# Kernel optimization log

Measured on AMD Instinct MI355X. Metric: run time of the kernel, lower is better.

Reference implementation:

```python
import jax, jax.numpy as jnp
import numpy as np

GENRES = 20; TAGS = 1000; GTAGS = 1128; MOVIES = 20000; YEARS = 120; TBINS = 128
B = 1024; HIST = 50; PH = 256; OD = 128
EG = 8; ET = 16; EGT = 16; EM = 32; EY = 8; EUG = 32; ETS = 4
PAD = MOVIES  # padding index; context buffers have MOVIES+1 rows, last row = zeros


def setup_inputs():
    ks = iter(jax.random.split(jax.random.key(0), 64))
    nrm = lambda shp, s=0.1: (s * jax.random.normal(next(ks), shp)).astype(jnp.float32)
    P = MOVIES + 1
    genome_ctx = jax.random.uniform(next(ks), (P, GTAGS), dtype=jnp.float32).at[-1].set(0.0)
    genre_ctx = jax.random.uniform(next(ks), (P, GENRES), dtype=jnp.float32).at[-1].set(0.0)
    tag_ctx = jax.random.uniform(next(ks), (P, TAGS), dtype=jnp.float32).at[-1].set(0.0)
    year_ctx = jax.random.randint(next(ks), (P,), 0, YEARS).at[-1].set(0)
    return dict(
        user_genre_contexts=jax.random.uniform(next(ks), (B, GENRES), dtype=jnp.float32),
        user_watch_history=jax.random.randint(next(ks), (B, HIST), 0, P),
        user_watch_history_ratings=5.0 * jax.random.uniform(next(ks), (B, HIST), dtype=jnp.float32),
        timestamps=jax.random.randint(next(ks), (B,), 0, TBINS),
        target_movieId=jax.random.randint(next(ks), (B,), 0, MOVIES),
        genome_ctx=genome_ctx, genre_ctx=genre_ctx, tag_ctx=tag_ctx, year_ctx=year_ctx,
        item_emb=nrm((P, EM), 0.01).at[-1].set(0.0),  # padding_idx row zeroed
        year_emb_tab=nrm((YEARS, EY), 0.01),
        ts_emb_tab=nrm((TBINS, ETS), 0.01),
        w_item=nrm((EM, EM)), b_item=jnp.zeros((EM,), jnp.float32),
        w_genre=nrm((GENRES, EG)), b_genre=jnp.zeros((EG,), jnp.float32),
        w_tag=nrm((TAGS, ET)), b_tag=jnp.zeros((ET,), jnp.float32),
        w_genome=nrm((GTAGS, EGT)), b_genome=jnp.zeros((EGT,), jnp.float32),
        w_year=nrm((EY, EY)), b_year=jnp.zeros((EY,), jnp.float32),
        w_ugenre=nrm((GENRES, EUG)), b_ugenre=jnp.zeros((EUG,), jnp.float32),
        w_ts=nrm((ETS, ETS)), b_ts=jnp.zeros((ETS,), jnp.float32),
        w_up1=nrm((OD + EGT + EUG + ETS, PH)), b_up1=jnp.zeros((PH,), jnp.float32),
        w_up2=nrm((PH, OD)), b_up2=jnp.zeros((OD,), jnp.float32),
        w_ip1=nrm((EG + ET + EGT + EM + EY, PH)), b_ip1=jnp.zeros((PH,), jnp.float32),
        w_ip2=nrm((PH, OD)), b_ip2=jnp.zeros((OD,), jnp.float32),
    )


def reference(user_genre_contexts, user_watch_history, user_watch_history_ratings,
              timestamps, target_movieId, genome_ctx, genre_ctx, tag_ctx, year_ctx,
              item_emb, year_emb_tab, ts_emb_tab,
              w_item, b_item, w_genre, b_genre, w_tag, b_tag, w_genome, b_genome,
              w_year, b_year, w_ugenre, b_ugenre, w_ts, b_ts,
              w_up1, b_up1, w_up2, b_up2, w_ip1, b_ip1, w_ip2, b_ip2):
    lt = lambda x, W, b: jnp.tanh(x @ W + b)

    def item_tower(mg, mt, mgt, yr, ids):
        # concat of five small Linear+Tanh towers, then 2-layer projection MLP
        cat = jnp.concatenate([
            lt(mg, w_genre, b_genre), lt(mt, w_tag, b_tag), lt(mgt, w_genome, b_genome),
            lt(item_emb[ids], w_item, b_item), lt(year_emb_tab[yr], w_year, b_year)], axis=-1)
        return jax.nn.relu(cat @ w_ip1 + b_ip1) @ w_ip2 + b_ip2

    Bn, Hn = user_watch_history.shape
    pad_mask = (user_watch_history != PAD).astype(jnp.float32)[..., None]       # (B,H,1)
    rating_weights = user_watch_history_ratings[..., None] * pad_mask            # (B,H,1)
    weight_sum = jnp.clip(jnp.abs(rating_weights).sum(axis=1), 1e-6)             # (B,1)

    # item pool: full item-tower embeddings of watched movies, rating-weighted avg
    flat = user_watch_history.reshape(-1)
    embs = item_tower(genre_ctx[flat], tag_ctx[flat], genome_ctx[flat],
                      year_ctx[flat], flat).reshape(Bn, Hn, OD)
    item_pool = (embs * rating_weights).sum(axis=1) / weight_sum                 # (B,OD)

    # genome pool (kept separately in use_item_pool_for_history mode)
    genome_embs = lt(genome_ctx[user_watch_history], w_genome, b_genome)         # (B,H,EGT)
    genome_emb = (genome_embs * rating_weights).sum(axis=1) / weight_sum

    genre_emb = lt(user_genre_contexts, w_ugenre, b_ugenre)
    ts_emb = lt(ts_emb_tab[timestamps], w_ts, b_ts)
    user_cat = jnp.concatenate([item_pool, genome_emb, genre_emb, ts_emb], axis=1)
    user = jax.nn.relu(user_cat @ w_up1 + b_up1) @ w_up2 + b_up2                 # (B,OD)

    item = item_tower(genre_ctx[target_movieId], tag_ctx[target_movieId],
                      genome_ctx[target_movieId], year_ctx[target_movieId], target_movieId)
    return jnp.einsum('bd,bd->b', user, item)
```

## Files before the change

kernel.cpp:

```cpp
#include <hip/hip_runtime.h>
#include <hip/hip_bf16.h>

typedef __bf16 bf16x8 __attribute__((ext_vector_type(8)));
typedef __bf16 bf16x4 __attribute__((ext_vector_type(4)));
typedef float  f32x4  __attribute__((ext_vector_type(4)));

namespace {
constexpr int P       = 20001;
constexpr int NT_TILE = 1251;
constexpr int PROWS   = NT_TILE * 16;
constexpr int NGENRES = 20;
constexpr int NTAGS   = 1000;
constexpr int NGTAGS  = 1128;
constexpr int NB      = 1024;
constexpr int NH      = 50;
constexpr int PHID    = 256;
constexpr int OD      = 128;
constexpr int EG = 8, ET = 16, EGT = 16, EM = 32, EY = 8, EUG = 32, ETS = 4;
constexpr int PAD  = 20000;
constexpr int SC   = 104;
constexpr int SH   = 264;
constexpr int UC   = 192;
constexpr int UCS  = 200;
constexpr int KC_TAG = 32, KC_GEN = 36;
constexpr int KC_IP1 = 3,  NT_IP1 = 16;
constexpr int KC_IP2 = 8,  NT_IP2 = 8;
constexpr int KC_UP1 = 6,  NT_UP1 = 16;
constexpr int KC_UP2 = 8,  NT_UP2 = 8;
}

static __device__ __forceinline__ f32x4 mfma16(bf16x8 a, bf16x8 b, f32x4 c) {
  return __builtin_amdgcn_mfma_f32_16x16x32_bf16(a, b, c, 0, 0, 0);
}

static __device__ __forceinline__ bf16x8 cvt8(float4 v0, float4 v1) {
  return (bf16x8){(__bf16)v0.x, (__bf16)v0.y, (__bf16)v0.z, (__bf16)v0.w,
                  (__bf16)v1.x, (__bf16)v1.y, (__bf16)v1.z, (__bf16)v1.w};
}

__global__ __launch_bounds__(512) void setup_wf_kernel(
    const float* __restrict__ w_tag, const float* __restrict__ w_genome,
    const float* __restrict__ w_ip1, const float* __restrict__ w_ip2,
    const float* __restrict__ w_up1, const float* __restrict__ w_up2,
    __bf16* __restrict__ Wtf, __bf16* __restrict__ Wgf,
    __bf16* __restrict__ Wip1f, __bf16* __restrict__ Wip2f,
    __bf16* __restrict__ Wup1f, __bf16* __restrict__ Wup2f)
{
  const int b = blockIdx.x, t = threadIdx.x;
  const int l = t >> 3, j = t & 7;
  const int krow = (l >> 4) * 8 + j, l15 = l & 15;
  const float* src; __bf16* dst; int K, N, kc, nt;
  if (b < 32)        { src = w_tag;    dst = Wtf   + (long)b * 512;       K = NTAGS;  N = 16;  kc = b;      nt = 0; }
  else if (b < 68)   { int i = b - 32;  src = w_genome; dst = Wgf   + (long)i * 512; K = NGTAGS; N = 16;  kc = i;      nt = 0; }
  else if (b < 116)  { int i = b - 68;  src = w_ip1;    dst = Wip1f + (long)i * 512; K = 80;     N = 256; kc = i / 16; nt = i % 16; }
  else if (b < 180)  { int i = b - 116; src = w_ip2;    dst = Wip2f + (long)i * 512; K = 256;    N = 128; kc = i / 8;  nt = i % 8; }
  else if (b < 276)  { int i = b - 180; src = w_up1;    dst = Wup1f + (long)i * 512; K = 180;    N = 256; kc = i / 16; nt = i % 16; }
  else               { int i = b - 276; src = w_up2;    dst = Wup2f + (long)i * 512; K = 256;    N = 128; kc = i / 8;  nt = i % 8; }
  const int k = kc * 32 + krow, n = nt * 16 + l15;
  float v = (k < K) ? src[(long)k * N + n] : 0.f;
  dst[t] = (__bf16)v;
}

__global__ __launch_bounds__(256, 3) void tower_kernel(
    const float* __restrict__ tag_ctx, const float* __restrict__ genome_ctx,
    const float* __restrict__ genre_ctx, const int* __restrict__ year_ctx,
    const float* __restrict__ item_emb, const float* __restrict__ year_tab,
    const float* __restrict__ w_genre, const float* __restrict__ b_genre,
    const float* __restrict__ b_tag,   const float* __restrict__ b_genome,
    const float* __restrict__ w_item,  const float* __restrict__ b_item,
    const float* __restrict__ w_year,  const float* __restrict__ b_year,
    const float* __restrict__ b_ip1,   const float* __restrict__ b_ip2,
    const __bf16* __restrict__ Wtf,   const __bf16* __restrict__ Wgf,
    const __bf16* __restrict__ Wip1f, const __bf16* __restrict__ Wip2f,
    float* __restrict__ T, float* __restrict__ GT)
{
  __shared__ __align__(16) __bf16 s_cat[16][SC];
  __shared__ __align__(16) __bf16 s_h[16][SH];
  __shared__ __align__(16) f32x4  s_redT[3][64];
  __shared__ __align__(16) f32x4  s_redG[3][64];

  const int t = threadIdx.x, tile = blockIdx.x;
  const int wave = t >> 6, lane = t & 63, l15 = lane & 15, quad = lane >> 4;
  const int r = t >> 4, c16 = t & 15;
  const long rid   = min(tile * 16 + l15, P - 1);
  const long rid_r = min(tile * 16 + r,   P - 1);

  const float* trow = tag_ctx    + rid * NTAGS;
  const float* grow = genome_ctx + rid * NGTAGS;

  float4 ta[16];
  float4 ga[18];
  {
    #pragma unroll
    for (int kc = 0; kc < 8; ++kc) {
      const int cc = min((wave * 8 + kc) * 32 + quad * 8, NTAGS - 8);
      ta[2 * kc]     = *(const float4*)(trow + cc);
      ta[2 * kc + 1] = *(const float4*)(trow + cc + 4);
    }
    #pragma unroll
    for (int kc = 0; kc < 9; ++kc) {
      const int cc = min((wave * 9 + kc) * 32 + quad * 8, NGTAGS - 8);
      ga[2 * kc]     = *(const float4*)(grow + cc);
      ga[2 * kc + 1] = *(const float4*)(grow + cc + 4);
    }
  }
  __builtin_amdgcn_sched_barrier(0);

  f32x4 accT = {0.f, 0.f, 0.f, 0.f};
  #pragma unroll
  for (int kc = 0; kc < 8; ++kc) {
    bf16x8 tb = *(const bf16x8*)(Wtf + ((long)(wave * 8 + kc) * 64 + lane) * 8);
    accT = mfma16(cvt8(ta[2 * kc], ta[2 * kc + 1]), tb, accT);
  }
  if (wave > 0) s_redT[wave - 1][lane] = accT;

  f32x4 accG = {0.f, 0.f, 0.f, 0.f};
  #pragma unroll
  for (int kc = 0; kc < 9; ++kc) {
    bf16x8 gb = *(const bf16x8*)(Wgf + ((long)(wave * 9 + kc) * 64 + lane) * 8);
    accG = mfma16(cvt8(ga[2 * kc], ga[2 * kc + 1]), gb, accG);
  }
  if (wave != 1) s_redG[wave ? wave - 1 : 0][lane] = accG;

  {
    const int m = r, j = c16;
    const long id = rid_r;
    if (j < 8) {
      const float* rg = genre_ctx + id * NGENRES;
      float a = b_genre[j];
      #pragma unroll
      for (int k = 0; k < NGENRES; ++k) a = fmaf(rg[k], w_genre[k * EG + j], a);
      s_cat[m][j] = (__bf16)tanhf(a);
      s_cat[m][80 + j] = (__bf16)0.f;
      s_cat[m][88 + j] = (__bf16)0.f;
    } else {
      const int jj = j - 8;
      const int yr = year_ctx[id];
      float a = b_year[jj];
      #pragma unroll
      for (int k = 0; k < EY; ++k)
        a = fmaf(year_tab[yr * EY + k], w_year[k * EY + jj], a);
      s_cat[m][72 + jj] = (__bf16)tanhf(a);
    }
    const float* e = item_emb + id * EM;
    float a0 = b_item[2 * j], a1 = b_item[2 * j + 1];
    #pragma unroll 8
    for (int k = 0; k < EM; ++k) {
      float ev = e[k];
      a0 = fmaf(ev, w_item[k * EM + 2 * j], a0);
      a1 = fmaf(ev, w_item[k * EM + 2 * j + 1], a1);
    }
    s_cat[m][40 + 2 * j]     = (__bf16)tanhf(a0);
    s_cat[m][40 + 2 * j + 1] = (__bf16)tanhf(a1);
  }
  __syncthreads();

  if (wave == 0) {
    accT += s_redT[0][lane]; accT += s_redT[1][lane]; accT += s_redT[2][lane];
    const float bt = b_tag[l15];
    #pragma unroll
    for (int r2 = 0; r2 < 4; ++r2)
      s_cat[quad * 4 + r2][EG + l15] = (__bf16)tanhf(accT[r2] + bt);
  } else if (wave == 1) {
    accG += s_redG[0][lane]; accG += s_redG[1][lane]; accG += s_redG[2][lane];
    const float bg = b_genome[l15];
    #pragma unroll
    for (int r2 = 0; r2 < 4; ++r2) {
      int m = quad * 4 + r2;
      float v = tanhf(accG[r2] + bg);
      s_cat[m][EG + ET + l15] = (__bf16)v;
      GT[(long)(tile * 16 + m) * EGT + l15] = v;
    }
  }
  __syncthreads();

  {
    bf16x8 af[KC_IP1];
    #pragma unroll
    for (int kc = 0; kc < KC_IP1; ++kc)
      af[kc] = *(const bf16x8*)&s_cat[l15][kc * 32 + quad * 8];
    #pragma unroll
    for (int nt = 0; nt < 4; ++nt) {
      const int n = wave * 64 + nt * 16 + l15;
      const float bb = b_ip1[n];
      f32x4 acc = {bb, bb, bb, bb};
      bf16x8 bfr[KC_IP1];
      #pragma unroll
      for (int kc = 0; kc < KC_IP1; ++kc)
        bfr[kc] = *(const bf16x8*)(Wip1f + ((long)(kc * NT_IP1 + wave * 4 + nt) * 64 + lane) * 8);
      #pragma unroll
      for (int kc = 0; kc < KC_IP1; ++kc)
        acc = mfma16(af[kc], bfr[kc], acc);
      #pragma unroll
      for (int r2 = 0; r2 < 4; ++r2)
        s_h[quad * 4 + r2][n] = (__bf16)fmaxf(acc[r2], 0.f);
    }
  }
  __syncthreads();

  {
    bf16x8 af[KC_IP2];
    #pragma unroll
    for (int kc = 0; kc < KC_IP2; ++kc)
      af[kc] = *(const bf16x8*)&s_h[l15][kc * 32 + quad * 8];
    #pragma unroll
    for (int nt = 0; nt < 2; ++nt) {
      const int n = wave * 32 + nt * 16 + l15;
      const float bb = b_ip2[n];
      f32x4 acc = {bb, bb, bb, bb};
      bf16x8 bfr[KC_IP2];
      #pragma unroll
      for (int kc = 0; kc < KC_IP2; ++kc)
        bfr[kc] = *(const bf16x8*)(Wip2f + ((long)(kc * NT_IP2 + wave * 2 + nt) * 64 + lane) * 8);
      #pragma unroll
      for (int kc = 0; kc < KC_IP2; ++kc)
        acc = mfma16(af[kc], bfr[kc], acc);
      #pragma unroll
      for (int r2 = 0; r2 < 4; ++r2)
        T[(long)(tile * 16 + quad * 4 + r2) * OD + n] = acc[r2];
    }
  }
}

__global__ __launch_bounds__(256) void user_pool_kernel(
    const float* __restrict__ ugc, const int* __restrict__ hist,
    const float* __restrict__ ratings, const int* __restrict__ tstamps,
    const float* __restrict__ ts_tab,
    const float* __restrict__ w_ugenre, const float* __restrict__ b_ugenre,
    const float* __restrict__ w_ts, const float* __restrict__ b_ts,
    const float* __restrict__ T, const float* __restrict__ GT,
    __bf16* __restrict__ Ucat)
{
  __shared__ float s_w[64];
  __shared__ int   s_ids[64];
  __shared__ float s_part[2][OD];
  __shared__ float s_gp[8][EGT];
  __shared__ float s_inv;

  const int b = blockIdx.x, t = threadIdx.x;

  if (t < 64) {
    int id = PAD; float w = 0.f;
    if (t < NH) {
      id = hist[b * NH + t];
      float r = ratings[b * NH + t];
      w = (id != PAD) ? r : 0.f;
    }
    s_ids[t] = id; s_w[t] = w;
    float s = fabsf(w);
    #pragma unroll
    for (int off = 32; off; off >>= 1) s += __shfl_xor(s, off, 64);
    if (t == 0) s_inv = 1.f / fmaxf(s, 1e-6f);
  }
  __syncthreads();
  const float inv = s_inv;

  {
    const int c = t & (OD - 1), part = t >> 7;
    float acc = 0.f;
    #pragma unroll
    for (int i = 0; i < 25; ++i) {
      const int h = part * 25 + i;
      acc = fmaf(s_w[h], T[(long)s_ids[h] * OD + c], acc);
    }
    s_part[part][c] = acc;
  }
  __syncthreads();
  if (t < OD) {
    Ucat[(long)b * UC + t] = (__bf16)((s_part[0][t] + s_part[1][t]) * inv);
  } else {
    const int uu = t - 128, col = uu & 15, part = uu >> 4;
    float acc = 0.f;
    #pragma unroll
    for (int i = 0; i < 7; ++i) {
      const int h = part * 7 + i;
      if (h < NH) acc = fmaf(s_w[h], GT[(long)s_ids[h] * EGT + col], acc);
    }
    s_gp[part][col] = acc;
  }
  __syncthreads();
  if (t < EGT) {
    float acc = 0.f;
    #pragma unroll
    for (int p = 0; p < 8; ++p) acc += s_gp[p][t];
    Ucat[(long)b * UC + OD + t] = (__bf16)(acc * inv);
  } else if (t >= 32 && t < 64) {
    const int j = t - 32;
    float a = b_ugenre[j];
    #pragma unroll
    for (int k = 0; k < NGENRES; ++k)
      a = fmaf(ugc[b * NGENRES + k], w_ugenre[k * EUG + j], a);
    Ucat[(long)b * UC + 144 + j] = (__bf16)tanhf(a);
  } else if (t >= 64 && t < 64 + ETS) {
    const int j = t - 64;
    const int ts = tstamps[b];
    float a = b_ts[j];
    #pragma unroll
    for (int k = 0; k < ETS; ++k)
      a = fmaf(ts_tab[ts * ETS + k], w_ts[k * ETS + j], a);
    Ucat[(long)b * UC + 176 + j] = (__bf16)tanhf(a);
  } else if (t >= 68 && t < 80) {
    Ucat[(long)b * UC + 180 + (t - 68)] = (__bf16)0.f;
  }
}

__global__ __launch_bounds__(256) void user_mlp_kernel(
    const int* __restrict__ target,
    const float* __restrict__ b_up1, const float* __restrict__ b_up2,
    const __bf16* __restrict__ Wup1f, const __bf16* __restrict__ Wup2f,
    const __bf16* __restrict__ Ucat, const float* __restrict__ T,
    float* __restrict__ out)
{
  __shared__ __align__(16) __bf16 s_u[16][UCS];
  __shared__ __align__(16) __bf16 s_h[16][SH];
  __shared__ __align__(16) float  s_e[16][132];
  __shared__ float s_red[2];

  const int t = threadIdx.x, blk = blockIdx.x;
  const int wave = t >> 6, lane = t & 63, l15 = lane & 15, quad = lane >> 4;
  const int u0 = blk * 16;

  {
    const int uu = t >> 4, s = t & 15;
    const __bf16* src = Ucat + (long)(u0 + uu) * UC;
    *(bf16x8*)&s_u[uu][s * 8] = *(const bf16x8*)(src + s * 8);
    if (s < 8)
      *(bf16x8*)&s_u[uu][(s + 16) * 8] = *(const bf16x8*)(src + (s + 16) * 8);
  }
  __syncthreads();

  {
    bf16x8 af[KC_UP1];
    #pragma unroll
    for (int kc = 0; kc < KC_UP1; ++kc)
      af[kc] = *(const bf16x8*)&s_u[l15][kc * 32 + quad * 8];
    #pragma unroll
    for (int nt = 0; nt < 4; ++nt) {
      const int n = wave * 64 + nt * 16 + l15;
      const float bb = b_up1[n];
      f32x4 acc = {bb, bb, bb, bb};
      bf16x8 bfr[KC_UP1];
      #pragma unroll
      for (int kc = 0; kc < KC_UP1; ++kc)
        bfr[kc] = *(const bf16x8*)(Wup1f + ((long)(kc * NT_UP1 + wave * 4 + nt) * 64 + lane) * 8);
      #pragma unroll
      for (int kc = 0; kc < KC_UP1; ++kc)
        acc = mfma16(af[kc], bfr[kc], acc);
      #pragma unroll
      for (int r2 = 0; r2 < 4; ++r2)
        s_h[quad * 4 + r2][n] = (__bf16)fmaxf(acc[r2], 0.f);
    }
  }
  __syncthreads();

  {
    bf16x8 af[KC_UP2];
    #pragma unroll
    for (int kc = 0; kc < KC_UP2; ++kc)
      af[kc] = *(const bf16x8*)&s_h[l15][kc * 32 + quad * 8];
    #pragma unroll
    for (int nt = 0; nt < 2; ++nt) {
      const int n = wave * 32 + nt * 16 + l15;
      const float bb = b_up2[n];
      f32x4 acc = {bb, bb, bb, bb};
      bf16x8 bfr[KC_UP2];
      #pragma unroll
      for (int kc = 0; kc < KC_UP2; ++kc)
        bfr[kc] = *(const bf16x8*)(Wup2f + ((long)(kc * NT_UP2 + wave * 2 + nt) * 64 + lane) * 8);
      #pragma unroll
      for (int kc = 0; kc < KC_UP2; ++kc)
        acc = mfma16(af[kc], bfr[kc], acc);
      #pragma unroll
      for (int r2 = 0; r2 < 4; ++r2)
        s_e[quad * 4 + r2][n] = acc[r2];
    }
  }
  __syncthreads();

  if (t < 128) {
    const int uu = t >> 3, q = t & 7;
    const int tgt = target[u0 + uu];
    const float* trow = T + (long)tgt * OD + q * 16;
    float s = 0.f;
    #pragma unroll
    for (int i = 0; i < 4; ++i) {
      float4 v = *(const float4*)(trow + i * 4);
      f32x4 e = *(const f32x4*)&s_e[uu][q * 16 + i * 4];
      s += v.x * e[0] + v.y * e[1] + v.z * e[2] + v.w * e[3];
    }
    s += __shfl_down(s, 1, 64);
    s += __shfl_down(s, 2, 64);
    s += __shfl_down(s, 4, 64);
    if (q == 0) out[u0 + uu] = s;
  }
  (void)s_red;
}

extern "C" void kernel_launch(void* const* d_in, const int* in_sizes, int n_in,
                              void* d_out, int out_size, void* d_ws, size_t ws_size,
                              hipStream_t stream) {
  const float* ugc      = (const float*)d_in[0];
  const int*   hist     = (const int*)  d_in[1];
  const float* ratings  = (const float*)d_in[2];
  const int*   tstamps  = (const int*)  d_in[3];
  const int*   target   = (const int*)  d_in[4];
  const float* genome   = (const float*)d_in[5];
  const float* genrec   = (const float*)d_in[6];
  const float* tagc     = (const float*)d_in[7];
  const int*   yearc    = (const int*)  d_in[8];
  const float* item_emb = (const float*)d_in[9];
  const float* year_tab = (const float*)d_in[10];
  const float* ts_tab   = (const float*)d_in[11];
  const float* w_item   = (const float*)d_in[12];
  const float* b_item   = (const float*)d_in[13];
  const float* w_genre  = (const float*)d_in[14];
  const float* b_genre  = (const float*)d_in[15];
  const float* w_tag    = (const float*)d_in[16];
  const float* b_tag    = (const float*)d_in[17];
  const float* w_genome = (const float*)d_in[18];
  const float* b_genome = (const float*)d_in[19];
  const float* w_year   = (const float*)d_in[20];
  const float* b_year   = (const float*)d_in[21];
  const float* w_ugenre = (const float*)d_in[22];
  const float* b_ugenre = (const float*)d_in[23];
  const float* w_ts     = (const float*)d_in[24];
  const float* b_ts     = (const float*)d_in[25];
  const float* w_up1    = (const float*)d_in[26];
  const float* b_up1    = (const float*)d_in[27];
  const float* w_up2    = (const float*)d_in[28];
  const float* b_up2    = (const float*)d_in[29];
  const float* w_ip1    = (const float*)d_in[30];
  const float* b_ip1    = (const float*)d_in[31];
  const float* w_ip2    = (const float*)d_in[32];
  const float* b_ip2    = (const float*)d_in[33];

  char* ws = (char*)d_ws;
  size_t off = 0;
  float*  T     = (float*) (ws + off); off += (size_t)PROWS * OD * 4;
  float*  GT    = (float*) (ws + off); off += (size_t)PROWS * EGT * 4;
  __bf16* Ucat  = (__bf16*)(ws + off); off += (size_t)NB * UC * 2;
  __bf16* Wtf   = (__bf16*)(ws + off); off += (size_t)KC_TAG * 512 * 2;
  __bf16* Wgf   = (__bf16*)(ws + off); off += (size_t)KC_GEN * 512 * 2;
  __bf16* Wip1f = (__bf16*)(ws + off); off += (size_t)KC_IP1 * NT_IP1 * 512 * 2;
  __bf16* Wip2f = (__bf16*)(ws + off); off += (size_t)KC_IP2 * NT_IP2 * 512 * 2;
  __bf16* Wup1f = (__bf16*)(ws + off); off += (size_t)KC_UP1 * NT_UP1 * 512 * 2;
  __bf16* Wup2f = (__bf16*)(ws + off); off += (size_t)KC_UP2 * NT_UP2 * 512 * 2;

  setup_wf_kernel<<<dim3(340), dim3(512), 0, stream>>>(
      w_tag, w_genome, w_ip1, w_ip2, w_up1, w_up2,
      Wtf, Wgf, Wip1f, Wip2f, Wup1f, Wup2f);

  tower_kernel<<<dim3(NT_TILE), dim3(256), 0, stream>>>(
      tagc, genome, genrec, yearc, item_emb, year_tab,
      w_genre, b_genre, b_tag, b_genome, w_item, b_item, w_year, b_year,
      b_ip1, b_ip2, Wtf, Wgf, Wip1f, Wip2f, T, GT);

  user_pool_kernel<<<dim3(NB), dim3(256), 0, stream>>>(
      ugc, hist, ratings, tstamps, ts_tab,
      w_ugenre, b_ugenre, w_ts, b_ts, T, GT, Ucat);

  user_mlp_kernel<<<dim3(NB / 16), dim3(256), 0, stream>>>(
      target, b_up1, b_up2, Wup1f, Wup2f, Ucat, T, (float*)d_out);
}
```

Measured before the change: 285.3 us.

## Stream tag/genome rows via global_load_lds with swizzled 4-stage LDS pipeline

Replaces the up-front register loads of tag and genome context rows in the tower kernel with direct global-to-LDS loads (global_load_lds) into a per-wave 4-slot staging buffer. A 3-deep software pipeline issues chunks ahead and waits on vmcnt before each MFMA, and an XOR swizzle keeps LDS reads conflict-free. This cuts VGPR pressure from holding 34 float4 values per thread and overlaps memory with compute, at the cost of 32KB extra LDS per block, which may reduce occupancy below the 3-blocks launch bound.

Measured after the change: 285.9 us. Within noise of the previous version (+0.2%).

```diff
diff --git a/kernel.cpp b/kernel.cpp
--- a/kernel.cpp
+++ b/kernel.cpp
@@ -38,6 +38,12 @@
                   (__bf16)v1.x, (__bf16)v1.y, (__bf16)v1.z, (__bf16)v1.w};
 }
 
+static __device__ __forceinline__ void gldlds(const void* g, void* l) {
+  __builtin_amdgcn_global_load_lds(
+      (const __attribute__((address_space(1))) void*)g,
+      (__attribute__((address_space(3))) void*)l, 16, 0, 0);
+}
+
 __global__ __launch_bounds__(512) void setup_wf_kernel(
     const float* __restrict__ w_tag, const float* __restrict__ w_genome,
     const float* __restrict__ w_ip1, const float* __restrict__ w_ip2,
@@ -74,6 +80,7 @@
     const __bf16* __restrict__ Wip1f, const __bf16* __restrict__ Wip2f,
     float* __restrict__ T, float* __restrict__ GT)
 {
+  __shared__ __align__(16) float  s_stage[4][4][512];
   __shared__ __align__(16) __bf16 s_cat[16][SC];
   __shared__ __align__(16) __bf16 s_h[16][SH];
   __shared__ __align__(16) f32x4  s_redT[3][64];
@@ -82,44 +89,74 @@
   const int t = threadIdx.x, tile = blockIdx.x;
   const int wave = t >> 6, lane = t & 63, l15 = lane & 15, quad = lane >> 4;
   const int r = t >> 4, c16 = t & 15;
-  const long rid   = min(tile * 16 + l15, P - 1);
   const long rid_r = min(tile * 16 + r,   P - 1);
 
-  const float* trow = tag_ctx    + rid * NTAGS;
-  const float* grow = genome_ctx + rid * NGTAGS;
-
-  float4 ta[16];
-  float4 ga[18];
-  {
-    #pragma unroll
-    for (int kc = 0; kc < 8; ++kc) {
-      const int cc = min((wave * 8 + kc) * 32 + quad * 8, NTAGS - 8);
-      ta[2 * kc]     = *(const float4*)(trow + cc);
-      ta[2 * kc + 1] = *(const float4*)(trow + cc + 4);
-    }
-    #pragma unroll
-    for (int kc = 0; kc < 9; ++kc) {
-      const int cc = min((wave * 9 + kc) * 32 + quad * 8, NGTAGS - 8);
-      ga[2 * kc]     = *(const float4*)(grow + cc);
-      ga[2 * kc + 1] = *(const float4*)(grow + cc + 4);
-    }
-  }
-  __builtin_amdgcn_sched_barrier(0);
+  const int rowd = lane >> 3;
+  const int swz  = (lane & 7) ^ (rowd & 7);
+  const long c16b = (long)swz * 16;
+  const long rid0 = min((long)tile * 16 + rowd,     (long)P - 1);
+  const long rid1 = min((long)tile * 16 + 8 + rowd, (long)P - 1);
+  const char* tg0 = (const char*)tag_ctx    + rid0 * (NTAGS  * 4);
+  const char* tg1 = (const char*)tag_ctx    + rid1 * (NTAGS  * 4);
+  const char* gg0 = (const char*)genome_ctx + rid0 * (NGTAGS * 4);
+  const char* gg1 = (const char*)genome_ctx + rid1 * (NGTAGS * 4);
+
+  const int rdo0 = l15 * 128 + (((quad * 2 + 0) ^ (l15 & 7)) * 16);
+  const int rdo1 = l15 * 128 + (((quad * 2 + 1) ^ (l15 & 7)) * 16);
+
+  bf16x8 bfr[17];
+  #pragma unroll
+  for (int mc = 0; mc < 8; ++mc)
+    bfr[mc] = *(const bf16x8*)(Wtf + ((long)(wave * 8 + mc) * 64 + lane) * 8);
+  #pragma unroll
+  for (int mc = 0; mc < 9; ++mc)
+    bfr[8 + mc] = *(const bf16x8*)(Wgf + ((long)(wave * 9 + mc) * 64 + lane) * 8);
+  #pragma unroll
+  for (int i = 0; i < 17; ++i) asm volatile("" :: "v"(bfr[i]));
+  asm volatile("s_waitcnt vmcnt(0)" ::: "memory");
 
   f32x4 accT = {0.f, 0.f, 0.f, 0.f};
-  #pragma unroll
-  for (int kc = 0; kc < 8; ++kc) {
-    bf16x8 tb = *(const bf16x8*)(Wtf + ((long)(wave * 8 + kc) * 64 + lane) * 8);
-    accT = mfma16(cvt8(ta[2 * kc], ta[2 * kc + 1]), tb, accT);
-  }
-  if (wave > 0) s_redT[wave - 1][lane] = accT;
-
   f32x4 accG = {0.f, 0.f, 0.f, 0.f};
-  #pragma unroll
-  for (int kc = 0; kc < 9; ++kc) {
-    bf16x8 gb = *(const bf16x8*)(Wgf + ((long)(wave * 9 + kc) * 64 + lane) * 8);
-    accG = mfma16(cvt8(ga[2 * kc], ga[2 * kc + 1]), gb, accG);
-  }
+
+#define ISSUE(MC) do {                                                         \
+    const int  mi_ = (MC);                                                     \
+    const bool isT_ = (mi_ < 8);                                               \
+    const long ko_  = isT_ ? (long)(wave * 8 + mi_) * 128                      \
+                           : (long)(wave * 9 + (mi_ - 8)) * 128;               \
+    const long lim_ = isT_ ? (long)996 * 4 : (long)1124 * 4;                   \
+    long off_ = ko_ + c16b; if (off_ > lim_) off_ = lim_;                      \
+    float* lp_ = &s_stage[wave][mi_ & 3][0];                                   \
+    gldlds((isT_ ? tg0 : gg0) + off_, lp_);                                    \
+    gldlds((isT_ ? tg1 : gg1) + off_, (char*)lp_ + 1024);                      \
+  } while (0)
+
+#define CONSUME(MC) do {                                                       \
+    const float* sp_ = &s_stage[wave][(MC) & 3][0];                            \
+    float4 a0_ = *(const float4*)((const char*)sp_ + rdo0);                    \
+    float4 a1_ = *(const float4*)((const char*)sp_ + rdo1);                    \
+    f32x4& ac_ = ((MC) < 8) ? accT : accG;                                     \
+    ac_ = mfma16(cvt8(a0_, a1_), bfr[(MC)], ac_);                              \
+  } while (0)
+
+#define STEP(MC, VM) {                                                         \
+    if ((MC) + 3 <= 16) ISSUE((MC) + 3);                                       \
+    asm volatile("s_waitcnt vmcnt(" #VM ")" ::: "memory");                     \
+    __builtin_amdgcn_sched_barrier(0);                                         \
+    CONSUME(MC);                                                               \
+  }
+
+  ISSUE(0); ISSUE(1); ISSUE(2);
+  STEP(0, 6)  STEP(1, 6)  STEP(2, 6)  STEP(3, 6)
+  STEP(4, 6)  STEP(5, 6)  STEP(6, 6)  STEP(7, 6)
+  STEP(8, 6)  STEP(9, 6)  STEP(10, 6) STEP(11, 6)
+  STEP(12, 6) STEP(13, 6) STEP(14, 4) STEP(15, 2)
+  STEP(16, 0)
+
+#undef STEP
+#undef CONSUME
+#undef ISSUE
+
+  if (wave > 0)  s_redT[wave - 1][lane] = accT;
   if (wave != 1) s_redG[wave ? wave - 1 : 0][lane] = accG;
 
   {
@@ -184,13 +221,13 @@
       const int n = wave * 64 + nt * 16 + l15;
       const float bb = b_ip1[n];
       f32x4 acc = {bb, bb, bb, bb};
-      bf16x8 bfr[KC_IP1];
+      bf16x8 bfr2[KC_IP1];
       #pragma unroll
       for (int kc = 0; kc < KC_IP1; ++kc)
-        bfr[kc] = *(const bf16x8*)(Wip1f + ((long)(kc * NT_IP1 + wave * 4 + nt) * 64 + lane) * 8);
+        bfr2[kc] = *(const bf16x8*)(Wip1f + ((long)(kc * NT_IP1 + wave * 4 + nt) * 64 + lane) * 8);
       #pragma unroll
       for (int kc = 0; kc < KC_IP1; ++kc)
-        acc = mfma16(af[kc], bfr[kc], acc);
+        acc = mfma16(af[kc], bfr2[kc], acc);
       #pragma unroll
       for (int r2 = 0; r2 < 4; ++r2)
         s_h[quad * 4 + r2][n] = (__bf16)fmaxf(acc[r2], 0.f);
@@ -208,13 +245,13 @@
       const int n = wave * 32 + nt * 16 + l15;
       const float bb = b_ip2[n];
       f32x4 acc = {bb, bb, bb, bb};
-      bf16x8 bfr[KC_IP2];
+      bf16x8 bfr2[KC_IP2];
       #pragma unroll
       for (int kc = 0; kc < KC_IP2; ++kc)
-        bfr[kc] = *(const bf16x8*)(Wip2f + ((long)(kc * NT_IP2 + wave * 2 + nt) * 64 + lane) * 8);
+        bfr2[kc] = *(const bf16x8*)(Wip2f + ((long)(kc * NT_IP2 + wave * 2 + nt) * 64 + lane) * 8);
       #pragma unroll
       for (int kc = 0; kc < KC_IP2; ++kc)
-        acc = mfma16(af[kc], bfr[kc], acc);
+        acc = mfma16(af[kc], bfr2[kc], acc);
       #pragma unroll
       for (int r2 = 0; r2 < 4; ++r2)
         T[(long)(tile * 16 + quad * 4 + r2) * OD + n] = acc[r2];
```

## Stage tag and genome context rows through LDS with direct global-to-LDS loads

Applied to the files above, without the earlier changes.

Replaces the per-thread register prefetch of tag and genome context rows in the tower kernel with global_load_lds transfers into an XOR-swizzled shared buffer. Each is done in two halves, with barriers, before the MFMA reduction. The genome weight packing is padded to 40 K-chunks to match the new split, and the occupancy hint drops from 3 to 2 blocks per SM. The aim is to cut register pressure and get coalesced row loads. The cost is extra synchronisation, less overlap between loads and MFMA, and a large LDS footprint per block.

New measurement: 284.7 us. Within noise of the previous version (-0.2%).

```diff
diff --git a/kernel.cpp b/kernel.cpp
--- a/kernel.cpp
+++ b/kernel.cpp
@@ -22,7 +22,8 @@
 constexpr int SH   = 264;
 constexpr int UC   = 192;
 constexpr int UCS  = 200;
-constexpr int KC_TAG = 32, KC_GEN = 36;
+constexpr int KC_TAG  = 32;
+constexpr int KC_GENF = 40;
 constexpr int KC_IP1 = 3,  NT_IP1 = 16;
 constexpr int KC_IP2 = 8,  NT_IP2 = 8;
 constexpr int KC_UP1 = 6,  NT_UP1 = 16;
@@ -36,6 +37,12 @@
 static __device__ __forceinline__ bf16x8 cvt8(float4 v0, float4 v1) {
   return (bf16x8){(__bf16)v0.x, (__bf16)v0.y, (__bf16)v0.z, (__bf16)v0.w,
                   (__bf16)v1.x, (__bf16)v1.y, (__bf16)v1.z, (__bf16)v1.w};
+}
+
+static __device__ __forceinline__ void gldlds(const void* g, void* l) {
+  __builtin_amdgcn_global_load_lds(
+      (const __attribute__((address_space(1))) void*)g,
+      (__attribute__((address_space(3))) void*)l, 16, 0, 0);
 }
 
 __global__ __launch_bounds__(512) void setup_wf_kernel(
@@ -51,17 +58,17 @@
   const int krow = (l >> 4) * 8 + j, l15 = l & 15;
   const float* src; __bf16* dst; int K, N, kc, nt;
   if (b < 32)        { src = w_tag;    dst = Wtf   + (long)b * 512;       K = NTAGS;  N = 16;  kc = b;      nt = 0; }
-  else if (b < 68)   { int i = b - 32;  src = w_genome; dst = Wgf   + (long)i * 512; K = NGTAGS; N = 16;  kc = i;      nt = 0; }
-  else if (b < 116)  { int i = b - 68;  src = w_ip1;    dst = Wip1f + (long)i * 512; K = 80;     N = 256; kc = i / 16; nt = i % 16; }
-  else if (b < 180)  { int i = b - 116; src = w_ip2;    dst = Wip2f + (long)i * 512; K = 256;    N = 128; kc = i / 8;  nt = i % 8; }
-  else if (b < 276)  { int i = b - 180; src = w_up1;    dst = Wup1f + (long)i * 512; K = 180;    N = 256; kc = i / 16; nt = i % 16; }
-  else               { int i = b - 276; src = w_up2;    dst = Wup2f + (long)i * 512; K = 256;    N = 128; kc = i / 8;  nt = i % 8; }
+  else if (b < 72)   { int i = b - 32;  src = w_genome; dst = Wgf   + (long)i * 512; K = NGTAGS; N = 16;  kc = i;      nt = 0; }
+  else if (b < 120)  { int i = b - 72;  src = w_ip1;    dst = Wip1f + (long)i * 512; K = 80;     N = 256; kc = i / 16; nt = i % 16; }
+  else if (b < 184)  { int i = b - 120; src = w_ip2;    dst = Wip2f + (long)i * 512; K = 256;    N = 128; kc = i / 8;  nt = i % 8; }
+  else if (b < 280)  { int i = b - 184; src = w_up1;    dst = Wup1f + (long)i * 512; K = 180;    N = 256; kc = i / 16; nt = i % 16; }
+  else               { int i = b - 280; src = w_up2;    dst = Wup2f + (long)i * 512; K = 256;    N = 128; kc = i / 8;  nt = i % 8; }
   const int k = kc * 32 + krow, n = nt * 16 + l15;
   float v = (k < K) ? src[(long)k * N + n] : 0.f;
   dst[t] = (__bf16)v;
 }
 
-__global__ __launch_bounds__(256, 3) void tower_kernel(
+__global__ __launch_bounds__(256, 2) void tower_kernel(
     const float* __restrict__ tag_ctx, const float* __restrict__ genome_ctx,
     const float* __restrict__ genre_ctx, const int* __restrict__ year_ctx,
     const float* __restrict__ item_emb, const float* __restrict__ year_tab,
@@ -74,6 +81,10 @@
     const __bf16* __restrict__ Wip1f, const __bf16* __restrict__ Wip2f,
     float* __restrict__ T, float* __restrict__ GT)
 {
+  __shared__ __align__(16) union {
+    char tag[16 * 128 * 16];
+    char gen[16 * 192 * 16];
+  } u;
   __shared__ __align__(16) __bf16 s_cat[16][SC];
   __shared__ __align__(16) __bf16 s_h[16][SH];
   __shared__ __align__(16) f32x4  s_redT[3][64];
@@ -82,44 +93,63 @@
   const int t = threadIdx.x, tile = blockIdx.x;
   const int wave = t >> 6, lane = t & 63, l15 = lane & 15, quad = lane >> 4;
   const int r = t >> 4, c16 = t & 15;
-  const long rid   = min(tile * 16 + l15, P - 1);
-  const long rid_r = min(tile * 16 + r,   P - 1);
-
-  const float* trow = tag_ctx    + rid * NTAGS;
-  const float* grow = genome_ctx + rid * NGTAGS;
-
-  float4 ta[16];
-  float4 ga[18];
-  {
-    #pragma unroll
-    for (int kc = 0; kc < 8; ++kc) {
-      const int cc = min((wave * 8 + kc) * 32 + quad * 8, NTAGS - 8);
-      ta[2 * kc]     = *(const float4*)(trow + cc);
-      ta[2 * kc + 1] = *(const float4*)(trow + cc + 4);
-    }
-    #pragma unroll
-    for (int kc = 0; kc < 9; ++kc) {
-      const int cc = min((wave * 9 + kc) * 32 + quad * 8, NGTAGS - 8);
-      ga[2 * kc]     = *(const float4*)(grow + cc);
-      ga[2 * kc + 1] = *(const float4*)(grow + cc + 4);
-    }
-  }
-  __builtin_amdgcn_sched_barrier(0);
+  const long rid_r = min(tile * 16 + r, P - 1);
+  const int x = l15 & 7;
 
   f32x4 accT = {0.f, 0.f, 0.f, 0.f};
+  f32x4 accG = {0.f, 0.f, 0.f, 0.f};
+
   #pragma unroll
-  for (int kc = 0; kc < 8; ++kc) {
-    bf16x8 tb = *(const bf16x8*)(Wtf + ((long)(wave * 8 + kc) * 64 + lane) * 8);
-    accT = mfma16(cvt8(ta[2 * kc], ta[2 * kc + 1]), tb, accT);
-  }
-  if (wave > 0) s_redT[wave - 1][lane] = accT;
-
-  f32x4 accG = {0.f, 0.f, 0.f, 0.f};
+  for (int h = 0; h < 2; ++h) {
+    #pragma unroll
+    for (int cc = 0; cc < 8; ++cc) {
+      const int c = wave * 8 + cc, rr = c >> 1, i = c & 1;
+      const long rid = min(tile * 16 + rr, P - 1);
+      const char* rp = (const char*)tag_ctx + rid * (NTAGS * 4);
+      const int gs = min(((i * 64 + lane) ^ (rr & 7)) + h * 128, 249);
+      gldlds(rp + (long)gs * 16, u.tag + ((rr * 128 + i * 64) * 16));
+    }
+    asm volatile("s_waitcnt vmcnt(0)" ::: "memory");
+    __syncthreads();
+    #pragma unroll
+    for (int c = 0; c < 4; ++c) {
+      const int kcg = h * 16 + wave * 4 + c;
+      const int j = (wave * 4 + c) * 8 + quad * 2;
+      const float4* rowp = (const float4*)u.tag + l15 * 128;
+      const float4 a0 = rowp[j ^ x];
+      const float4 a1 = rowp[(j + 1) ^ x];
+      bf16x8 tb = *(const bf16x8*)(Wtf + ((long)kcg * 64 + lane) * 8);
+      accT = mfma16(cvt8(a0, a1), tb, accT);
+    }
+    __syncthreads();
+  }
+
   #pragma unroll
-  for (int kc = 0; kc < 9; ++kc) {
-    bf16x8 gb = *(const bf16x8*)(Wgf + ((long)(wave * 9 + kc) * 64 + lane) * 8);
-    accG = mfma16(cvt8(ga[2 * kc], ga[2 * kc + 1]), gb, accG);
-  }
+  for (int h = 0; h < 2; ++h) {
+    #pragma unroll
+    for (int cc = 0; cc < 12; ++cc) {
+      const int c = wave * 12 + cc, rr = c / 3, i = c % 3;
+      const long rid = min(tile * 16 + rr, P - 1);
+      const char* rp = (const char*)genome_ctx + rid * (NGTAGS * 4);
+      const int gs = min(((i * 64 + lane) ^ (rr & 7)) + h * 160, 281);
+      gldlds(rp + (long)gs * 16, u.gen + ((rr * 192 + i * 64) * 16));
+    }
+    asm volatile("s_waitcnt vmcnt(0)" ::: "memory");
+    __syncthreads();
+    #pragma unroll
+    for (int c = 0; c < 5; ++c) {
+      const int kcg = h * 20 + wave * 5 + c;
+      const int j = (wave * 5 + c) * 8 + quad * 2;
+      const float4* rowp = (const float4*)u.gen + l15 * 192;
+      const float4 a0 = rowp[j ^ x];
+      const float4 a1 = rowp[(j + 1) ^ x];
+      bf16x8 gb = *(const bf16x8*)(Wgf + ((long)kcg * 64 + lane) * 8);
+      accG = mfma16(cvt8(a0, a1), gb, accG);
+    }
+    __syncthreads();
+  }
+
+  if (wave > 0)  s_redT[wave - 1][lane] = accT;
   if (wave != 1) s_redG[wave ? wave - 1 : 0][lane] = accG;
 
   {
@@ -314,7 +344,6 @@
   __shared__ __align__(16) __bf16 s_u[16][UCS];
   __shared__ __align__(16) __bf16 s_h[16][SH];
   __shared__ __align__(16) float  s_e[16][132];
-  __shared__ float s_red[2];
 
   const int t = threadIdx.x, blk = blockIdx.x;
   const int wave = t >> 6, lane = t & 63, l15 = lane & 15, quad = lane >> 4;
@@ -393,7 +422,6 @@
     s += __shfl_down(s, 4, 64);
     if (q == 0) out[u0 + uu] = s;
   }
-  (void)s_red;
 }
 
 extern "C" void kernel_launch(void* const* d_in, const int* in_sizes, int n_in,
@@ -439,14 +467,14 @@
   float*  T     = (float*) (ws + off); off += (size_t)PROWS * OD * 4;
   float*  GT    = (float*) (ws + off); off += (size_t)PROWS * EGT * 4;
   __bf16* Ucat  = (__bf16*)(ws + off); off += (size_t)NB * UC * 2;
-  __bf16* Wtf   = (__bf16*)(ws + off); off += (size_t)KC_TAG * 512 * 2;
-  __bf16* Wgf   = (__bf16*)(ws + off); off += (size_t)KC_GEN * 512 * 2;
+  __bf16* Wtf   = (__bf16*)(ws + off); off += (size_t)KC_TAG  * 512 * 2;
+  __bf16* Wgf   = (__bf16*)(ws + off); off += (size_t)KC_GENF * 512 * 2;
   __bf16* Wip1f = (__bf16*)(ws + off); off += (size_t)KC_IP1 * NT_IP1 * 512 * 2;
   __bf16* Wip2f = (__bf16*)(ws + off); off += (size_t)KC_IP2 * NT_IP2 * 512 * 2;
   __bf16* Wup1f = (__bf16*)(ws + off); off += (size_t)KC_UP1 * NT_UP1 * 512 * 2;
   __bf16* Wup2f = (__bf16*)(ws + off); off += (size_t)KC_UP2 * NT_UP2 * 512 * 2;
 
-  setup_wf_kernel<<<dim3(340), dim3(512), 0, stream>>>(
+  setup_wf_kernel<<<dim3(344), dim3(512), 0, stream>>>(
       w_tag, w_genome, w_ip1, w_ip2, w_up1, w_up2,
       Wtf, Wgf, Wip1f, Wip2f, Wup1f, Wup2f);
 
```
